# Optimization experiments

Hardware: AMD Instinct MI355X
Metric: run time of the kernel (lower is better)

Reference implementation:

```python
import jax, jax.numpy as jnp
import numpy as np

N_EMBD = 1024
HEAD_SIZE = 64


def setup_inputs() -> dict:
    key = jax.random.key(0)
    k1, k2, k3, k4 = jax.random.split(key, 4)
    x = jax.random.normal(k1, (8, 2048, N_EMBD), dtype=jnp.float32)
    # torch Linear(n_embd, head_size, bias=False): y = x @ W.T with W [out,in].
    # Store as [in, out] so y = x @ W. Scale init like torch default (~1/sqrt(in)).
    s = 1.0 / np.sqrt(N_EMBD)
    Wk = jax.random.uniform(k2, (N_EMBD, HEAD_SIZE), jnp.float32, -s, s)
    Wq = jax.random.uniform(k3, (N_EMBD, HEAD_SIZE), jnp.float32, -s, s)
    Wv = jax.random.uniform(k4, (N_EMBD, HEAD_SIZE), jnp.float32, -s, s)
    return {"x": x, "Wk": Wk, "Wq": Wq, "Wv": Wv}


def reference(x, Wk, Wq, Wv):
    # x: [B,T,C]
    B, T, C = x.shape
    k = x @ Wk  # [B,T,H]
    q = x @ Wq  # [B,T,H]
    v = x @ Wv  # [B,T,H]
    scale = HEAD_SIZE ** -0.5
    wei = jnp.einsum('bth,bsh->bts', q, k) * scale  # [B,T,T]
    causal = jnp.tril(jnp.ones((T, T), dtype=bool))  # [T,T]
    wei = jnp.where(causal[None, :, :], wei, -jnp.inf)
    wei = jax.nn.softmax(wei, axis=-1)
    # dropout(p=0.2) is identity in eval mode (deterministic baseline)
    out = jnp.einsum('bts,bsh->bth', wei, v)  # [B,T,H]
    return out
```

## Files before the change

kernel.cpp:

```cpp
#include <hip/hip_runtime.h>
#include <hip/hip_bf16.h>

#define B_DIM 8
#define T_DIM 2048
#define C_DIM 1024
#define H_DIM 64
#define BT (B_DIM * T_DIM)

typedef __attribute__((ext_vector_type(8))) short bf16x8;
typedef __attribute__((ext_vector_type(4))) float f32x4;

__device__ __forceinline__ ushort f2bf(float f) {
    __hip_bfloat16 h = __float2bfloat16(f);
    return *reinterpret_cast<ushort*>(&h);
}
__device__ __forceinline__ unsigned int packbf(float a, float b) {
    return (unsigned int)f2bf(a) | ((unsigned int)f2bf(b) << 16);
}

__global__ __launch_bounds__(256) void wt_convert_kernel(
    const float* __restrict__ Wk, const float* __restrict__ Wq,
    const float* __restrict__ Wv, ushort* __restrict__ wt)
{
    const int n = blockIdx.x;
    const float* src = (n < 64) ? Wk : (n < 128) ? Wq : Wv;
    const float scale = (n >= 64 && n < 128) ? 0.125f * 1.4426950408889634f : 1.0f;
    const int col = n & 63;
    for (int k = threadIdx.x; k < C_DIM; k += 256)
        wt[(size_t)n * C_DIM + k] = f2bf(src[(size_t)k * H_DIM + col] * scale);
}

__global__ __launch_bounds__(256) void qkv_gemm_kernel(
    const float* __restrict__ x, const ushort* __restrict__ wt,
    ushort* __restrict__ kb, ushort* __restrict__ qb, ushort* __restrict__ vt)
{
    __shared__ ushort Xf[2 * 2 * 64 * 8];
    __shared__ ushort Wf[12 * 2 * 64 * 8];
    const int tid = threadIdx.x;
    const int wave = tid >> 6, lane = tid & 63;
    const int col = lane & 15, quad = lane >> 4;
    const int r0 = blockIdx.x * 32;

    f32x4 acc[2][3];
    #pragma unroll
    for (int m = 0; m < 2; ++m)
        #pragma unroll
        for (int i = 0; i < 3; ++i) acc[m][i] = (f32x4){0.f, 0.f, 0.f, 0.f};

    const int xrow = (wave >> 1) * 16 + col;
    const int xcc  = (wave & 1) * 4 + quad;
    const float* xsrc = x + (size_t)(r0 + xrow) * C_DIM + xcc * 8;
    ushort* xdst = &Xf[(wave * 64 + lane) * 8];

    for (int k0 = 0; k0 < C_DIM; k0 += 64) {
        __syncthreads();
        {
            const float4 f0 = *(const float4*)(xsrc + k0);
            const float4 f1 = *(const float4*)(xsrc + k0 + 4);
            uint4 u;
            u.x = packbf(f0.x, f0.y); u.y = packbf(f0.z, f0.w);
            u.z = packbf(f1.x, f1.y); u.w = packbf(f1.z, f1.w);
            *(uint4*)xdst = u;
        }
        #pragma unroll
        for (int it = 0; it < 6; ++it) {
            const int r = it * 4 + wave;
            const int n  = (r >> 1) * 16 + col;
            const int cc = (r & 1) * 4 + quad;
            const uint4 u = *(const uint4*)(wt + (size_t)n * C_DIM + k0 + cc * 8);
            *(uint4*)&Wf[((size_t)r * 64 + lane) * 8] = u;
        }
        __syncthreads();
        #pragma unroll
        for (int ks = 0; ks < 2; ++ks) {
            const bf16x8 a0 = *(const bf16x8*)&Xf[((    ks) * 64 + lane) * 8];
            const bf16x8 a1 = *(const bf16x8*)&Xf[((2 + ks) * 64 + lane) * 8];
            #pragma unroll
            for (int i = 0; i < 3; ++i) {
                const bf16x8 b = *(const bf16x8*)
                    &Wf[(((wave * 3 + i) * 2 + ks) * 64 + lane) * 8];
                acc[0][i] = __builtin_amdgcn_mfma_f32_16x16x32_bf16(a0, b, acc[0][i], 0, 0, 0);
                acc[1][i] = __builtin_amdgcn_mfma_f32_16x16x32_bf16(a1, b, acc[1][i], 0, 0, 0);
            }
        }
    }

    #pragma unroll
    for (int i = 0; i < 3; ++i) {
        const int nt = wave * 3 + i;
        #pragma unroll
        for (int mf = 0; mf < 2; ++mf) {
            const int rbase = r0 + mf * 16 + quad * 4;
            if (nt < 4) {
                const int n = nt * 16 + col;
                #pragma unroll
                for (int r = 0; r < 4; ++r)
                    kb[(size_t)(rbase + r) * H_DIM + n] = f2bf(acc[mf][i][r]);
            } else if (nt < 8) {
                const int n = nt * 16 + col - 64;
                #pragma unroll
                for (int r = 0; r < 4; ++r)
                    qb[(size_t)(rbase + r) * H_DIM + n] = f2bf(acc[mf][i][r]);
            } else {
                const int h = nt * 16 + col - 128;
                const int vbatch = rbase >> 11, vrow = rbase & (T_DIM - 1);
                ushort u4[4] = {f2bf(acc[mf][i][0]), f2bf(acc[mf][i][1]),
                                f2bf(acc[mf][i][2]), f2bf(acc[mf][i][3])};
                unsigned long long uu; __builtin_memcpy(&uu, u4, 8);
                *(unsigned long long*)(vt + ((size_t)vbatch * H_DIM + h) * T_DIM + vrow) = uu;
            }
        }
    }
}

__global__ __launch_bounds__(256) void attn_kernel(
    const ushort* __restrict__ kb, const ushort* __restrict__ qb,
    const ushort* __restrict__ vt, float* __restrict__ out)
{
    __shared__ unsigned int Ps[4][16 * 34];
    __shared__ float Om[4][64][17];
    __shared__ float Mm[4][16], Lm[4][16];

    const int tid = threadIdx.x;
    const int wave = tid >> 6, lane = tid & 63;
    const int col = lane & 15, quad = lane >> 4;
    const int batch = blockIdx.x & 7;
    const int qtile = 127 - (blockIdx.x >> 3);
    const int q0 = qtile * 16;

    const ushort* kbase = kb + (size_t)batch * T_DIM * H_DIM;
    const ushort* vbase = vt + (size_t)batch * H_DIM * T_DIM;

    const size_t qoff = (size_t)(batch * T_DIM + q0 + col) * H_DIM + quad * 8;
    const bf16x8 bq0 = *(const bf16x8*)(qb + qoff);
    const bf16x8 bq1 = *(const bf16x8*)(qb + qoff + 32);

    float m_ = -INFINITY, l_ = 0.f;
    f32x4 o_[4];
    #pragma unroll
    for (int i = 0; i < 4; ++i) o_[i] = (f32x4){0.f, 0.f, 0.f, 0.f};

    const int ntiles = (q0 + 16 + 63) >> 6;
    unsigned int* psw = &Ps[wave][0];

    for (int t = wave; t < ntiles; t += 4) {
        const int kb0 = t * 64;
        f32x4 s[4];
        #pragma unroll
        for (int mt = 0; mt < 4; ++mt) s[mt] = (f32x4){0.f, 0.f, 0.f, 0.f};
        #pragma unroll
        for (int ks = 0; ks < 2; ++ks) {
            const bf16x8 bq = ks ? bq1 : bq0;
            #pragma unroll
            for (int mt = 0; mt < 4; ++mt) {
                const bf16x8 ak = *(const bf16x8*)
                    (kbase + (size_t)(kb0 + mt * 16 + col) * H_DIM + ks * 32 + quad * 8);
                s[mt] = __builtin_amdgcn_mfma_f32_16x16x32_bf16(ak, bq, s[mt], 0, 0, 0);
            }
        }
        if (kb0 + 63 > q0) {
            const int kq = kb0 + quad * 4 - q0 - col;
            #pragma unroll
            for (int mt = 0; mt < 4; ++mt)
                #pragma unroll
                for (int reg = 0; reg < 4; ++reg)
                    if (kq + mt * 16 + reg > 0) s[mt][reg] = -INFINITY;
        }
        float mr = -INFINITY;
        #pragma unroll
        for (int mt = 0; mt < 4; ++mt)
            #pragma unroll
            for (int reg = 0; reg < 4; ++reg) mr = fmaxf(mr, s[mt][reg]);
        mr = fmaxf(mr, __shfl_xor(mr, 16));
        mr = fmaxf(mr, __shfl_xor(mr, 32));
        const float mn = fmaxf(m_, mr);
        const float corr = exp2f(m_ - mn);
        float sum = 0.f;
        #pragma unroll
        for (int mt = 0; mt < 4; ++mt)
            #pragma unroll
            for (int reg = 0; reg < 4; ++reg) {
                const float pv = exp2f(s[mt][reg] - mn);
                s[mt][reg] = pv;
                sum += pv;
            }
        sum += __shfl_xor(sum, 16);
        sum += __shfl_xor(sum, 32);
        l_ = l_ * corr + sum;
        m_ = mn;
        #pragma unroll
        for (int ht = 0; ht < 4; ++ht) o_[ht] *= corr;
        #pragma unroll
        for (int mt = 0; mt < 4; ++mt) {
            uint2 w2;
            w2.x = packbf(s[mt][0], s[mt][1]);
            w2.y = packbf(s[mt][2], s[mt][3]);
            *(uint2*)&psw[col * 34 + mt * 8 + quad * 2] = w2;
        }
        #pragma unroll
        for (int ks2 = 0; ks2 < 2; ++ks2) {
            const uint2 ra = *(const uint2*)&psw[col * 34 + ks2 * 16 + quad * 4];
            const uint2 rb = *(const uint2*)&psw[col * 34 + ks2 * 16 + quad * 4 + 2];
            unsigned int ub[4] = {ra.x, ra.y, rb.x, rb.y};
            bf16x8 bp; __builtin_memcpy(&bp, ub, 16);
            #pragma unroll
            for (int ht = 0; ht < 4; ++ht) {
                const bf16x8 av = *(const bf16x8*)
                    (vbase + (size_t)(ht * 16 + col) * T_DIM + kb0 + ks2 * 32 + quad * 8);
                o_[ht] = __builtin_amdgcn_mfma_f32_16x16x32_bf16(av, bp, o_[ht], 0, 0, 0);
            }
        }
    }

    #pragma unroll
    for (int ht = 0; ht < 4; ++ht)
        #pragma unroll
        for (int reg = 0; reg < 4; ++reg)
            Om[wave][ht * 16 + quad * 4 + reg][col] = o_[ht][reg];
    if (lane < 16) { Mm[wave][lane] = m_; Lm[wave][lane] = l_; }
    __syncthreads();
    {
        const int q = tid >> 4, hb = tid & 15;
        const float M = fmaxf(fmaxf(Mm[0][q], Mm[1][q]), fmaxf(Mm[2][q], Mm[3][q]));
        const float a0 = exp2f(Mm[0][q] - M), a1 = exp2f(Mm[1][q] - M);
        const float a2 = exp2f(Mm[2][q] - M), a3 = exp2f(Mm[3][q] - M);
        const float L = Lm[0][q] * a0 + Lm[1][q] * a1 + Lm[2][q] * a2 + Lm[3][q] * a3;
        const float rL = 1.0f / L;
        float* orow = out + (size_t)(batch * T_DIM + q0 + q) * H_DIM;
        #pragma unroll
        for (int i = 0; i < 4; ++i) {
            const int h = hb + 16 * i;
            orow[h] = (Om[0][h][q] * a0 + Om[1][h][q] * a1 +
                       Om[2][h][q] * a2 + Om[3][h][q] * a3) * rL;
        }
    }
}

extern "C" void kernel_launch(void* const* d_in, const int* in_sizes, int n_in,
                              void* d_out, int out_size, void* d_ws, size_t ws_size,
                              hipStream_t stream)
{
    const float* x  = (const float*)d_in[0];
    const float* Wk = (const float*)d_in[1];
    const float* Wq = (const float*)d_in[2];
    const float* Wv = (const float*)d_in[3];

    ushort* kbuf = (ushort*)d_ws;
    ushort* qbuf = kbuf + (size_t)BT * H_DIM;
    ushort* vtb  = qbuf + (size_t)BT * H_DIM;
    ushort* wt   = vtb  + (size_t)BT * H_DIM;

    wt_convert_kernel<<<192, 256, 0, stream>>>(Wk, Wq, Wv, wt);
    qkv_gemm_kernel<<<BT / 32, 256, 0, stream>>>(x, wt, kbuf, qbuf, vtb);
    attn_kernel<<<B_DIM * 128, 256, 0, stream>>>(kbuf, qbuf, vtb, (float*)d_out);
}
```

Baseline: 161.2 us.

## Double-buffer QKV GEMM X tile and load weight fragments directly into registers

The QKV projection GEMM now loads each wave's weight fragments straight from global memory into registers instead of staging them through shared memory. The X tile is double-buffered in LDS, with the next k-step's loads issued before the current MFMAs, and only one barrier per iteration. This targets load latency and the cost of two syncs per step in the projection kernel, at the price of higher register pressure. It only affects the projection stage, not the attention kernel.

```diff
diff --git a/kernel.cpp b/kernel.cpp
--- a/kernel.cpp
+++ b/kernel.cpp
@@ -34,8 +34,7 @@
     const float* __restrict__ x, const ushort* __restrict__ wt,
     ushort* __restrict__ kb, ushort* __restrict__ qb, ushort* __restrict__ vt)
 {
-    __shared__ ushort Xf[2 * 2 * 64 * 8];
-    __shared__ ushort Wf[12 * 2 * 64 * 8];
+    __shared__ ushort Xf[2][4 * 64 * 8];
     const int tid = threadIdx.x;
     const int wave = tid >> 6, lane = tid & 63;
     const int col = lane & 15, quad = lane >> 4;
@@ -50,39 +49,67 @@
     const int xrow = (wave >> 1) * 16 + col;
     const int xcc  = (wave & 1) * 4 + quad;
     const float* xsrc = x + (size_t)(r0 + xrow) * C_DIM + xcc * 8;
-    ushort* xdst = &Xf[(wave * 64 + lane) * 8];
-
-    for (int k0 = 0; k0 < C_DIM; k0 += 64) {
+
+    const ushort* wsrc[3][2];
+    #pragma unroll
+    for (int j = 0; j < 3; ++j)
+        #pragma unroll
+        for (int ks = 0; ks < 2; ++ks)
+            wsrc[j][ks] = wt + (size_t)((wave * 3 + j) * 16 + col) * C_DIM
+                             + ks * 32 + quad * 8;
+
+    {
+        const float4 f0 = *(const float4*)(xsrc);
+        const float4 f1 = *(const float4*)(xsrc + 4);
+        uint4 u;
+        u.x = packbf(f0.x, f0.y); u.y = packbf(f0.z, f0.w);
+        u.z = packbf(f1.x, f1.y); u.w = packbf(f1.z, f1.w);
+        *(uint4*)&Xf[0][(wave * 64 + lane) * 8] = u;
+    }
+    bf16x8 wcur[3][2];
+    #pragma unroll
+    for (int j = 0; j < 3; ++j)
+        #pragma unroll
+        for (int ks = 0; ks < 2; ++ks)
+            wcur[j][ks] = *(const bf16x8*)(wsrc[j][ks]);
+    __syncthreads();
+
+    for (int i = 0; i < 16; ++i) {
+        const int b = i & 1;
+        bf16x8 wnxt[3][2];
+        float4 nf0, nf1;
+        if (i < 15) {
+            const int k1 = (i + 1) * 64;
+            #pragma unroll
+            for (int j = 0; j < 3; ++j)
+                #pragma unroll
+                for (int ks = 0; ks < 2; ++ks)
+                    wnxt[j][ks] = *(const bf16x8*)(wsrc[j][ks] + k1);
+            nf0 = *(const float4*)(xsrc + k1);
+            nf1 = *(const float4*)(xsrc + k1 + 4);
+        }
+        #pragma unroll
+        for (int ks = 0; ks < 2; ++ks) {
+            const bf16x8 a0 = *(const bf16x8*)&Xf[b][((    ks) * 64 + lane) * 8];
+            const bf16x8 a1 = *(const bf16x8*)&Xf[b][((2 + ks) * 64 + lane) * 8];
+            #pragma unroll
+            for (int j = 0; j < 3; ++j) {
+                acc[0][j] = __builtin_amdgcn_mfma_f32_16x16x32_bf16(a0, wcur[j][ks], acc[0][j], 0, 0, 0);
+                acc[1][j] = __builtin_amdgcn_mfma_f32_16x16x32_bf16(a1, wcur[j][ks], acc[1][j], 0, 0, 0);
+            }
+        }
+        if (i < 15) {
+            #pragma unroll
+            for (int j = 0; j < 3; ++j)
+                #pragma unroll
+                for (int ks = 0; ks < 2; ++ks)
+                    wcur[j][ks] = wnxt[j][ks];
+            uint4 u;
+            u.x = packbf(nf0.x, nf0.y); u.y = packbf(nf0.z, nf0.w);
+            u.z = packbf(nf1.x, nf1.y); u.w = packbf(nf1.z, nf1.w);
+            *(uint4*)&Xf[b ^ 1][(wave * 64 + lane) * 8] = u;
+        }
         __syncthreads();
-        {
-            const float4 f0 = *(const float4*)(xsrc + k0);
-            const float4 f1 = *(const float4*)(xsrc + k0 + 4);
-            uint4 u;
-            u.x = packbf(f0.x, f0.y); u.y = packbf(f0.z, f0.w);
-            u.z = packbf(f1.x, f1.y); u.w = packbf(f1.z, f1.w);
-            *(uint4*)xdst = u;
-        }
-        #pragma unroll
-        for (int it = 0; it < 6; ++it) {
-            const int r = it * 4 + wave;
-            const int n  = (r >> 1) * 16 + col;
-            const int cc = (r & 1) * 4 + quad;
-            const uint4 u = *(const uint4*)(wt + (size_t)n * C_DIM + k0 + cc * 8);
-            *(uint4*)&Wf[((size_t)r * 64 + lane) * 8] = u;
-        }
-        __syncthreads();
-        #pragma unroll
-        for (int ks = 0; ks < 2; ++ks) {
-            const bf16x8 a0 = *(const bf16x8*)&Xf[((    ks) * 64 + lane) * 8];
-            const bf16x8 a1 = *(const bf16x8*)&Xf[((2 + ks) * 64 + lane) * 8];
-            #pragma unroll
-            for (int i = 0; i < 3; ++i) {
-                const bf16x8 b = *(const bf16x8*)
-                    &Wf[(((wave * 3 + i) * 2 + ks) * 64 + lane) * 8];
-                acc[0][i] = __builtin_amdgcn_mfma_f32_16x16x32_bf16(a0, b, acc[0][i], 0, 0, 0);
-                acc[1][i] = __builtin_amdgcn_mfma_f32_16x16x32_bf16(a1, b, acc[1][i], 0, 0, 0);
-            }
-        }
     }
 
     #pragma unroll
```

Result: faster. 156.4 us (-3.0%).
